# Kernel tuning notes

Hardware: AMD Instinct MI355X
Metric: run time of the kernel (lower is better)

## Reference

```python
import jax, jax.numpy as jnp
import numpy as np

BS, NA, NC, G = 64, 3, 80, 44
IMG = 352
STRIDE = IMG / G  # 8.0
ANCHORS = np.array([[10.0, 13.0], [16.0, 30.0], [33.0, 23.0]], dtype=np.float32)
SCALED_ANCHORS = ANCHORS / STRIDE  # anchors in grid units


def setup_inputs() -> dict:
    key = jax.random.key(0)
    x = jax.random.normal(key, (BS, NA * (5 + NC), G, G), dtype=jnp.float32)
    return {"x": x}


def reference(x):
    bs = x.shape[0]
    # [bs, nA, 5+nC, H, W] -> [bs, nA, H, W, 5+nC]
    pred = x.reshape(bs, NA, 5 + NC, G, G).transpose(0, 1, 3, 4, 2)
    px = jax.nn.sigmoid(pred[..., 0])
    py = jax.nn.sigmoid(pred[..., 1])
    pw = pred[..., 2]
    ph = pred[..., 3]
    conf = jax.nn.sigmoid(pred[..., 4])
    pred_cls = jax.nn.sigmoid(pred[..., 5:])

    grid = jnp.arange(G, dtype=jnp.float32)
    grid_x = grid[None, None, None, :]          # broadcast over W
    grid_y = grid[None, None, :, None]          # broadcast over H
    aw = jnp.asarray(SCALED_ANCHORS[:, 0])[None, :, None, None]
    ah = jnp.asarray(SCALED_ANCHORS[:, 1])[None, :, None, None]

    bx = px + grid_x
    by = py + grid_y
    bw = jnp.exp(pw) * aw
    bh = jnp.exp(ph) * ah
    pred_boxes = jnp.stack([bx, by, bw, bh], axis=-1)  # [bs,nA,H,W,4]

    out = jnp.concatenate(
        [
            pred_boxes.reshape(bs, -1, 4) * jnp.float32(STRIDE),
            conf.reshape(bs, -1, 1),
            pred_cls.reshape(bs, -1, NC),
        ],
        axis=-1,
    )  # [bs, nA*G*G, 5+nC]
    return out
```

## Files before the change

kernel.cpp:

```cpp
#include <hip/hip_runtime.h>


#define BSZ      64
#define NA       3
#define NC       80
#define GRID     44
#define SPATIAL  (GRID * GRID)
#define CH       (5 + NC)
#define TILE     64
#define TILES_PER_BA ((SPATIAL + TILE - 1) / TILE)
#define NF       (CH * (TILE / 4))
#define NITER    ((NF + 255) / 256)
#define STRIDE_F 8.0f
#define NXCD     8
#define NWG      (BSZ * NA * TILES_PER_BA)
#define CHUNK    (NWG / NXCD)

typedef float vfloat4 __attribute__((ext_vector_type(4)));

__device__ __forceinline__ float sigf(float x) {
    return 1.0f / (1.0f + __expf(-x));
}

__global__ __launch_bounds__(256, 4)
void yolo_kernel(const float* __restrict__ in, float* __restrict__ out) {
    __shared__ float tile[TILE * CH];

    const int bid0 = blockIdx.x;
    const int bid  = (bid0 % NXCD) * CHUNK + bid0 / NXCD;

    const int t   = bid % TILES_PER_BA;
    const int ba  = bid / TILES_PER_BA;
    const int a   = ba % NA;

    const int s0    = t * TILE;
    const int valid = min(TILE, SPATIAL - s0);

    const float aw = (a == 0) ? 10.0f : (a == 1) ? 16.0f : 33.0f;
    const float ah = (a == 0) ? 13.0f : (a == 1) ? 30.0f : 23.0f;

    const int tid = threadIdx.x;
    const float* inbase = in + (size_t)ba * CH * SPATIAL + s0;

    float4 v[NITER];
    #pragma unroll
    for (int i = 0; i < NITER; ++i) {
        int f = tid + i * 256;
        int c = f >> 4, q = f & 15;
        if (f < NF && q * 4 < valid)
            v[i] = *(const float4*)(inbase + (size_t)c * SPATIAL + q * 4);
    }

    #pragma unroll
    for (int i = 0; i < NITER; ++i) {
        int f = tid + i * 256;
        int c = f >> 4, q = f & 15;
        if (f >= NF || q * 4 >= valid) continue;
        float r[4] = {v[i].x, v[i].y, v[i].z, v[i].w};
        #pragma unroll
        for (int j = 0; j < 4; ++j) {
            int   sl = q * 4 + j;
            int   gs = s0 + sl;
            float x  = r[j];
            float o;
            if (c == 0)      o = (sigf(x) + (float)(gs % GRID)) * STRIDE_F;
            else if (c == 1) o = (sigf(x) + (float)(gs / GRID)) * STRIDE_F;
            else if (c == 2) o = __expf(x) * aw;
            else if (c == 3) o = __expf(x) * ah;
            else             o = sigf(x);
            tile[sl * CH + c] = o;
        }
    }
    __syncthreads();

    const size_t obase = ((size_t)ba * SPATIAL + s0) * CH;
    const int total = valid * CH;
    for (int k4 = tid * 4; k4 < total; k4 += 1024) {
        vfloat4 w = *(const vfloat4*)(tile + k4);
        __builtin_nontemporal_store(w, (vfloat4*)(out + obase + k4));
    }
}

extern "C" void kernel_launch(void* const* d_in, const int* in_sizes, int n_in,
                              void* d_out, int out_size, void* d_ws, size_t ws_size,
                              hipStream_t stream) {
    const float* in = (const float*)d_in[0];
    float* out = (float*)d_out;
    yolo_kernel<<<NWG, 256, 0, stream>>>(in, out);
}
```

Baseline: 223.0 us.

## Give each wave its own tile slice and prefetch the next tile's loads

Each wave now handles its own 16-position slice of a tile and writes only its own LDS region, which removes the block-wide barrier. Each block walks four consecutive tiles and issues the next tile's global loads into a second register buffer before transforming and storing the current one, so memory latency overlaps with compute. The launch bound is raised to 7 blocks per CU and the grid shrinks by a factor of four. In exchange, each channel row is read as a 64-byte segment instead of 256 bytes, and register pressure rises from holding two load buffers.

```diff
diff --git a/kernel.cpp b/kernel.cpp
--- a/kernel.cpp
+++ b/kernel.cpp
@@ -8,13 +8,13 @@
 #define SPATIAL  (GRID * GRID)
 #define CH       (5 + NC)
 #define TILE     64
-#define TILES_PER_BA ((SPATIAL + TILE - 1) / TILE)
-#define NF       (CH * (TILE / 4))
-#define NITER    ((NF + 255) / 256)
+#define TPB      31
+#define NTL      (BSZ * NA * TPB)
+#define NT       4
+#define NBLK     (NTL / NT)
+#define NXCD     8
+#define CHUNKB   (NBLK / NXCD)
 #define STRIDE_F 8.0f
-#define NXCD     8
-#define NWG      (BSZ * NA * TILES_PER_BA)
-#define CHUNK    (NWG / NXCD)
 
 typedef float vfloat4 __attribute__((ext_vector_type(4)));
 
@@ -22,62 +22,105 @@
     return 1.0f / (1.0f + __expf(-x));
 }
 
-__global__ __launch_bounds__(256, 4)
-void yolo_kernel(const float* __restrict__ in, float* __restrict__ out) {
-    __shared__ float tile[TILE * CH];
+struct TileCtx { int s0, valid, ba; float aw, ah; };
 
-    const int bid0 = blockIdx.x;
-    const int bid  = (bid0 % NXCD) * CHUNK + bid0 / NXCD;
+__device__ __forceinline__ TileCtx tctx(int T) {
+    TileCtx tc;
+    int t   = T % TPB;
+    tc.ba   = T / TPB;
+    tc.s0   = t * TILE;
+    tc.valid = min(TILE, SPATIAL - tc.s0);
+    int a = tc.ba % NA;
+    tc.aw = (a == 0) ? 10.0f : (a == 1) ? 16.0f : 33.0f;
+    tc.ah = (a == 0) ? 13.0f : (a == 1) ? 30.0f : 23.0f;
+    return tc;
+}
 
-    const int t   = bid % TILES_PER_BA;
-    const int ba  = bid / TILES_PER_BA;
-    const int a   = ba % NA;
+__device__ __forceinline__ void issue_loads(const float* __restrict__ in,
+                                            const TileCtx& tc, int w, int l,
+                                            float4 (&v)[6]) {
+    const bool wact = (16 * w < tc.valid);
+    const float* ib = in + (size_t)tc.ba * CH * SPATIAL + tc.s0 + 16 * w;
+    #pragma unroll
+    for (int i = 0; i < 6; ++i) {
+        int p = i * 64 + l;
+        int c = p >> 2, ql = p & 3;
+        if (wact && p < 340)
+            v[i] = *(const float4*)(ib + (size_t)c * SPATIAL + 4 * ql);
+    }
+}
 
-    const int s0    = t * TILE;
-    const int valid = min(TILE, SPATIAL - s0);
-
-    const float aw = (a == 0) ? 10.0f : (a == 1) ? 16.0f : 33.0f;
-    const float ah = (a == 0) ? 13.0f : (a == 1) ? 30.0f : 23.0f;
-
-    const int tid = threadIdx.x;
-    const float* inbase = in + (size_t)ba * CH * SPATIAL + s0;
-
-    float4 v[NITER];
+__device__ __forceinline__ void transform(const TileCtx& tc, int w, int l,
+                                          const float4 (&v)[6],
+                                          float* __restrict__ wlds) {
+    const bool wact = (16 * w < tc.valid);
     #pragma unroll
-    for (int i = 0; i < NITER; ++i) {
-        int f = tid + i * 256;
-        int c = f >> 4, q = f & 15;
-        if (f < NF && q * 4 < valid)
-            v[i] = *(const float4*)(inbase + (size_t)c * SPATIAL + q * 4);
-    }
-
-    #pragma unroll
-    for (int i = 0; i < NITER; ++i) {
-        int f = tid + i * 256;
-        int c = f >> 4, q = f & 15;
-        if (f >= NF || q * 4 >= valid) continue;
+    for (int i = 0; i < 6; ++i) {
+        int p = i * 64 + l;
+        int c = p >> 2, ql = p & 3;
+        if (!wact || p >= 340) continue;
         float r[4] = {v[i].x, v[i].y, v[i].z, v[i].w};
         #pragma unroll
         for (int j = 0; j < 4; ++j) {
-            int   sl = q * 4 + j;
-            int   gs = s0 + sl;
+            int   sl = ql * 4 + j;
+            int   gs = tc.s0 + 16 * w + 4 * ql + j;
             float x  = r[j];
             float o;
             if (c == 0)      o = (sigf(x) + (float)(gs % GRID)) * STRIDE_F;
             else if (c == 1) o = (sigf(x) + (float)(gs / GRID)) * STRIDE_F;
-            else if (c == 2) o = __expf(x) * aw;
-            else if (c == 3) o = __expf(x) * ah;
+            else if (c == 2) o = __expf(x) * tc.aw;
+            else if (c == 3) o = __expf(x) * tc.ah;
             else             o = sigf(x);
-            tile[sl * CH + c] = o;
+            wlds[sl * CH + c] = o;
         }
     }
-    __syncthreads();
+}
 
-    const size_t obase = ((size_t)ba * SPATIAL + s0) * CH;
-    const int total = valid * CH;
-    for (int k4 = tid * 4; k4 < total; k4 += 1024) {
-        vfloat4 w = *(const vfloat4*)(tile + k4);
-        __builtin_nontemporal_store(w, (vfloat4*)(out + obase + k4));
+__device__ __forceinline__ void flush(float* __restrict__ out,
+                                      const TileCtx& tc, int w, int l,
+                                      const float* __restrict__ wlds) {
+    if (16 * w >= tc.valid) return;
+    const size_t ob = ((size_t)tc.ba * SPATIAL + tc.s0 + 16 * w) * (size_t)CH;
+    #pragma unroll
+    for (int i = 0; i < 6; ++i) {
+        int k = i * 256 + 4 * l;
+        if (k < 16 * CH) {
+            vfloat4 x = *(const vfloat4*)(wlds + k);
+            __builtin_nontemporal_store(x, (vfloat4*)(out + ob + k));
+        }
+    }
+}
+
+__global__ __launch_bounds__(256, 7)
+void yolo_kernel(const float* __restrict__ in, float* __restrict__ out) {
+    __shared__ float lds[4 * 16 * CH];
+
+    const int bid0 = blockIdx.x;
+    const int bid  = (bid0 % NXCD) * CHUNKB + bid0 / NXCD;
+    const int tid  = threadIdx.x;
+    const int w    = tid >> 6, l = tid & 63;
+    float* wlds = lds + w * 16 * CH;
+
+    const int T0 = bid * NT;
+    float4 vA[6], vB[6];
+
+    TileCtx tc = tctx(T0);
+    issue_loads(in, tc, w, l, vA);
+
+    #pragma unroll
+    for (int k = 0; k < NT; ++k) {
+        TileCtx tn;
+        if (k + 1 < NT) {
+            tn = tctx(T0 + k + 1);
+            issue_loads(in, tn, w, l, vB);
+        }
+        transform(tc, w, l, vA, wlds);
+        flush(out, tc, w, l, wlds);
+        if (k + 1 < NT) {
+            tc = tn;
+            #pragma unroll
+            for (int i = 0; i < 6; ++i) vA[i] = vB[i];
+        }
     }
 }
 
@@ -86,5 +129,5 @@
                               hipStream_t stream) {
     const float* in = (const float*)d_in[0];
     float* out = (float*)d_out;
-    yolo_kernel<<<NWG, 256, 0, stream>>>(in, out);
+    yolo_kernel<<<NBLK, 256, 0, stream>>>(in, out);
 }
```

Result: slower. 233.4 us (+4.6%).
